# Kernel tuning notes

Hardware: AMD Instinct MI355X
Metric: run time of the kernel (lower is better)

The kernel has to match this reference:

```python
import jax, jax.numpy as jnp
import numpy as np

B, N, C, G, K = 4, 6000, 91, 32, 100
IMG = 800.0
SCORE_TH = 0.05
NMS_TH = 0.5
MATCH_TH = 0.5
MIN_SIZE = 0.01
BBOX_CLIP = float(np.log(1000.0 / 16.0))
WX, WY, WW, WH = 10.0, 10.0, 5.0, 5.0


def _make_boxes(key, shape_prefix):
    k1, k2 = jax.random.split(key)
    xy = jax.random.uniform(k1, shape_prefix + (2,), minval=0.0, maxval=IMG - 130.0)
    wh = jax.random.uniform(k2, shape_prefix + (2,), minval=8.0, maxval=128.0)
    return jnp.concatenate([xy, xy + wh], axis=-1)


def setup_inputs() -> dict:
    key = jax.random.key(0)
    k1, k2, k3, k4, k5 = jax.random.split(key, 5)
    return {
        "class_logits": 2.0 * jax.random.normal(k1, (B * N, C), dtype=jnp.float32),
        "box_regression": jax.random.normal(k2, (B * N, C * 4), dtype=jnp.float32),
        "proposals": _make_boxes(k3, (B, N)),
        "gt_boxes": _make_boxes(k4, (B, G)),
        "gt_labels": jax.random.randint(k5, (B, G), 1, C),
    }


def _box_iou(a, b):
    # a [G,4], b [N,4] -> [G,N]
    area_a = (a[:, 2] - a[:, 0]) * (a[:, 3] - a[:, 1])
    area_b = (b[:, 2] - b[:, 0]) * (b[:, 3] - b[:, 1])
    lt = jnp.maximum(a[:, None, :2], b[None, :, :2])
    rb = jnp.minimum(a[:, None, 2:], b[None, :, 2:])
    wh = jnp.clip(rb - lt, 0.0)
    inter = wh[..., 0] * wh[..., 1]
    return inter / (area_a[:, None] + area_b[None, :] - inter)


def _decode(rel, props):
    # torchvision BoxCoder.decode; rel [N,C,4], props [N,4]
    w = props[:, 2] - props[:, 0]
    h = props[:, 3] - props[:, 1]
    cx = props[:, 0] + 0.5 * w
    cy = props[:, 1] + 0.5 * h
    dx = rel[..., 0] / WX
    dy = rel[..., 1] / WY
    dw = jnp.minimum(rel[..., 2] / WW, BBOX_CLIP)
    dh = jnp.minimum(rel[..., 3] / WH, BBOX_CLIP)
    pcx = dx * w[:, None] + cx[:, None]
    pcy = dy * h[:, None] + cy[:, None]
    pw = jnp.exp(dw) * w[:, None]
    ph = jnp.exp(dh) * h[:, None]
    return jnp.stack([pcx - 0.5 * pw, pcy - 0.5 * ph, pcx + 0.5 * pw, pcy + 0.5 * ph], axis=-1)


def _image(logits, reg, props, gtb, gtl):
    # --- assign_targets_to_proposals (Matcher, low=high=0.5, no low-quality matches) ---
    iou = _box_iou(gtb, props)                      # [G, N]
    best = iou.max(axis=0)
    mi = jnp.argmax(iou, axis=0)
    matched = jnp.where(best >= MATCH_TH, mi, -1)   # -1 == BELOW_LOW_THRESHOLD
    assigned = jnp.where(matched >= 0, gtl[jnp.clip(matched, 0)], 0)

    # --- postprocess_detections ---
    scores = jax.nn.softmax(logits, axis=-1)[:, 1:].reshape(-1)                       # [N*(C-1)]
    boxes = jnp.clip(_decode(reg.reshape(N, C, 4), props)[:, 1:], 0.0, IMG)
    boxes = boxes.reshape(-1, 4)                                                      # [N*(C-1),4]
    labels = jnp.tile(jnp.arange(1, C), N)                                            # [N*(C-1)]
    ws = boxes[:, 2] - boxes[:, 0]
    hs = boxes[:, 3] - boxes[:, 1]
    valid = (scores > SCORE_TH) & (ws >= MIN_SIZE) & (hs >= MIN_SIZE)
    s0 = jnp.where(valid, scores, -jnp.inf)
    # batched_nms trick: offset boxes by label so cross-class IoU is 0
    off = boxes + (labels.astype(boxes.dtype) * (IMG + 1.0))[:, None]
    off_area = (off[:, 2] - off[:, 0]) * (off[:, 3] - off[:, 1])

    def step(s, _):
        i = jnp.argmax(s)
        sc = s[i]
        b = off[i]
        lt = jnp.maximum(off[:, :2], b[:2])
        rb = jnp.minimum(off[:, 2:], b[2:])
        wh = jnp.clip(rb - lt, 0.0)
        inter = wh[:, 0] * wh[:, 1]
        iou_all = inter / (off_area + (b[2] - b[0]) * (b[3] - b[1]) - inter)
        s = jnp.where(iou_all > NMS_TH, -jnp.inf, s)  # suppress (includes self)
        ok = jnp.isfinite(sc)
        ob = jnp.where(ok, boxes[i], 0.0)
        osc = jnp.where(ok, sc, 0.0)
        ol = jnp.where(ok, labels[i], -1)
        return s, (ob, osc, ol)

    _, (kb, ksc, kl) = jax.lax.scan(step, s0, None, length=K)
    return kb, ksc, kl, assigned, matched


def reference(class_logits, box_regression, proposals, gt_boxes, gt_labels):
    logits = class_logits.reshape(B, N, C)
    reg = box_regression.reshape(B, N, C * 4)
    kb, ksc, kl, assigned, matched = jax.vmap(_image)(logits, reg, proposals, gt_boxes, gt_labels)
    dets = jnp.concatenate([kb, ksc[..., None]], axis=-1)  # [B, K, 5]
    return dets, kl, assigned, matched
```

## Files before the change

kernel.cpp:

```cpp
#include <hip/hip_runtime.h>
#include <math.h>

#define NB 4
#define NN 6000
#define NC 91
#define NG 32
#define NK 100
#define NCLS (NC - 1)
#define NBUC (NB * NCLS)
#define SLOTS_MAX 2048
#define CUR_STRIDE 32
#define PMAX 512
#define MPB 4096
#define RS_BLOCKS 6000

#define SCORE_TH 0.05f
#define NMS_TH 0.5f
#define MATCH_TH 0.5f
#define MIN_SIZE 0.01f
#define BBOX_CLIP 4.135166556742356f
#define C_SUP 0.5000000298023223876953125

__device__ __forceinline__ bool decode_one(
    const float* __restrict__ reg, const float* __restrict__ props,
    float l, float m, float s0, int row, int c, float out[5])
{
    float score = __fdiv_rn(expf(__fsub_rn(l, m)), s0);

    const float4 p = *reinterpret_cast<const float4*>(props + (size_t)row * 4);
    float w  = __fsub_rn(p.z, p.x);
    float h  = __fsub_rn(p.w, p.y);
    float cx = __fadd_rn(p.x, __fmul_rn(0.5f, w));
    float cy = __fadd_rn(p.y, __fmul_rn(0.5f, h));

    const float4 r4 = *reinterpret_cast<const float4*>(
        reg + (size_t)row * (NC * 4) + (size_t)c * 4);
    float dx = __fdiv_rn(r4.x, 10.0f);
    float dy = __fdiv_rn(r4.y, 10.0f);
    float dw = fminf(__fdiv_rn(r4.z, 5.0f), BBOX_CLIP);
    float dh = fminf(__fdiv_rn(r4.w, 5.0f), BBOX_CLIP);

    float pcx = __fadd_rn(__fmul_rn(dx, w), cx);
    float pcy = __fadd_rn(__fmul_rn(dy, h), cy);
    float pw  = __fmul_rn(expf(dw), w);
    float ph  = __fmul_rn(expf(dh), h);

    float x1 = __fsub_rn(pcx, __fmul_rn(0.5f, pw));
    float y1 = __fsub_rn(pcy, __fmul_rn(0.5f, ph));
    float x2 = __fadd_rn(pcx, __fmul_rn(0.5f, pw));
    float y2 = __fadd_rn(pcy, __fmul_rn(0.5f, ph));
    x1 = fminf(fmaxf(x1, 0.0f), 800.0f);
    y1 = fminf(fmaxf(y1, 0.0f), 800.0f);
    x2 = fminf(fmaxf(x2, 0.0f), 800.0f);
    y2 = fminf(fmaxf(y2, 0.0f), 800.0f);

    out[0] = score; out[1] = x1; out[2] = y1; out[3] = x2; out[4] = y2;
    float ws_ = __fsub_rn(x2, x1);
    float hs_ = __fsub_rn(y2, y1);
    return (score > SCORE_TH) && (ws_ >= MIN_SIZE) && (hs_ >= MIN_SIZE);
}

__global__ __launch_bounds__(256) void fused_kernel(
    const float* __restrict__ logits, const float* __restrict__ reg,
    const float* __restrict__ props, const float* __restrict__ gtb,
    const int* __restrict__ gtl,
    float* __restrict__ out_assigned, float* __restrict__ out_matched,
    int* __restrict__ cursors,
    float* __restrict__ e_sc, float* __restrict__ e_x1,
    float* __restrict__ e_y1, float* __restrict__ e_x2,
    float* __restrict__ e_y2, float* __restrict__ e_id, int slots)
{
    int bid = blockIdx.x;
    if (bid < RS_BLOCKS) {
        int wid = threadIdx.x >> 6, lane = threadIdx.x & 63;
        int row = bid * 4 + wid;
        const float* rp = logits + (size_t)row * NC;
        float l0 = rp[lane];
        float l1 = (lane < NC - 64) ? rp[64 + lane] : -INFINITY;
        float m = fmaxf(fmaxf(-INFINITY, l0), l1);
        for (int o = 32; o; o >>= 1) m = fmaxf(m, __shfl_down(m, o));
        m = __shfl(m, 0);
        float s = __fadd_rn(__fadd_rn(0.0f, expf(__fsub_rn(l0, m))),
                            expf(__fsub_rn(l1, m)));
        for (int o = 32; o; o >>= 1) s = __fadd_rn(s, __shfl_down(s, o));
        float s0 = __shfl(s, 0);
        float thr = __fadd_rn(m, logf(__fmul_rn(0.04f, s0)));

        int b = row / NN;
        int nprop = row - b * NN;

        if (lane >= 1 && l0 > thr) {
            float o[5];
            if (decode_one(reg, props, l0, m, s0, row, lane, o)) {
                int c = lane;
                int g = b * NCLS + (c - 1);
                int pos = atomicAdd(&cursors[g * CUR_STRIDE], 1);
                if (pos < slots) {
                    size_t idx = (size_t)g * slots + pos;
                    e_sc[idx] = o[0]; e_x1[idx] = o[1]; e_y1[idx] = o[2];
                    e_x2[idx] = o[3]; e_y2[idx] = o[4];
                    e_id[idx] = (float)(nprop * NCLS + (c - 1));
                }
            }
        }
        if (lane < NC - 64 && l1 > thr) {
            float o[5];
            int c = lane + 64;
            if (decode_one(reg, props, l1, m, s0, row, c, o)) {
                int g = b * NCLS + (c - 1);
                int pos = atomicAdd(&cursors[g * CUR_STRIDE], 1);
                if (pos < slots) {
                    size_t idx = (size_t)g * slots + pos;
                    e_sc[idx] = o[0]; e_x1[idx] = o[1]; e_y1[idx] = o[2];
                    e_x2[idx] = o[3]; e_y2[idx] = o[4];
                    e_id[idx] = (float)(nprop * NCLS + (c - 1));
                }
            }
        }
    } else {
        int t = (bid - RS_BLOCKS) * 256 + threadIdx.x;
        if (t >= NB * NN) return;
        int b = t / NN;
        const float4 p = *reinterpret_cast<const float4*>(props + (size_t)t * 4);
        float parea = __fmul_rn(__fsub_rn(p.z, p.x), __fsub_rn(p.w, p.y));
        float best = -1.0f; int bi = -1;
        for (int g = 0; g < NG; ++g) {
            const float4 q = *reinterpret_cast<const float4*>(gtb + ((size_t)b * NG + g) * 4);
            float garea = __fmul_rn(__fsub_rn(q.z, q.x), __fsub_rn(q.w, q.y));
            float ltx = fmaxf(q.x, p.x), lty = fmaxf(q.y, p.y);
            float rbx = fminf(q.z, p.z), rby = fminf(q.w, p.w);
            float wx = fmaxf(__fsub_rn(rbx, ltx), 0.0f);
            float wy = fmaxf(__fsub_rn(rby, lty), 0.0f);
            float inter = __fmul_rn(wx, wy);
            float iou = __fdiv_rn(inter, __fsub_rn(__fadd_rn(garea, parea), inter));
            if (iou > best) { best = iou; bi = g; }
        }
        int matched = (best >= MATCH_TH) ? bi : -1;
        int assigned = (matched >= 0) ? gtl[b * NG + matched] : 0;
        out_matched[t]  = (float)matched;
        out_assigned[t] = (float)assigned;
    }
}

__device__ void nms_glb(int g, int n, float* __restrict__ SC,
                        const float* __restrict__ X1, const float* __restrict__ Y1,
                        const float* __restrict__ X2, const float* __restrict__ Y2,
                        const float* __restrict__ ID, float tb, float cls,
                        float* __restrict__ selbuf, int* __restrict__ selcnt)
{
    int lane = threadIdx.x;
    int kout = 0;
    for (int k = 0; k < NK; ++k) {
        float bv = -INFINITY, boi = INFINITY; int bi = -1;
        for (int i = lane; i < n; i += 64) {
            float v = SC[i], oi = ID[i];
            if (v > bv || (v == bv && oi < boi)) { bv = v; boi = oi; bi = i; }
        }
        int wl = lane;
        for (int o = 1; o < 64; o <<= 1) {
            float v2 = __shfl_xor(bv, o); float o2 = __shfl_xor(boi, o);
            int l2 = __shfl_xor(wl, o);
            bool bt = (v2 > bv) || (v2 == bv && o2 < boi);
            bv = bt ? v2 : bv; boi = bt ? o2 : boi; wl = bt ? l2 : wl;
        }
        if (bv == -INFINITY) break;
        int wi = __shfl(bi, wl);
        float sx1 = X1[wi], sy1 = Y1[wi], sx2 = X2[wi], sy2 = Y2[wi];
        if (lane == wl) {
            float* so = selbuf + ((size_t)g * NK + k) * 8;
            so[0] = bv; so[1] = sx1; so[2] = sy1; so[3] = sx2; so[4] = sy2;
            so[5] = cls; so[6] = boi; so[7] = 0.0f;
        }
        float bx1 = __fadd_rn(sx1, tb), by1 = __fadd_rn(sy1, tb);
        float bx2 = __fadd_rn(sx2, tb), by2 = __fadd_rn(sy2, tb);
        float sar = __fmul_rn(__fsub_rn(bx2, bx1), __fsub_rn(by2, by1));
        for (int i = lane; i < n; i += 64) {
            float v = SC[i];
            if (v == -INFINITY) continue;
            float ox1 = __fadd_rn(X1[i], tb), oy1 = __fadd_rn(Y1[i], tb);
            float ox2 = __fadd_rn(X2[i], tb), oy2 = __fadd_rn(Y2[i], tb);
            float oar = __fmul_rn(__fsub_rn(ox2, ox1), __fsub_rn(oy2, oy1));
            float ltx = fmaxf(ox1, bx1), lty = fmaxf(oy1, by1);
            float rbx = fminf(ox2, bx2), rby = fminf(oy2, by2);
            float wx = fmaxf(__fsub_rn(rbx, ltx), 0.0f);
            float wy = fmaxf(__fsub_rn(rby, lty), 0.0f);
            float inter = __fmul_rn(wx, wy);
            float den = __fsub_rn(__fadd_rn(oar, sar), inter);
            if ((double)inter > C_SUP * (double)den) SC[i] = -INFINITY;
        }
        kout = k + 1;
    }
    if (lane == 0) selcnt[g] = kout;
}

template <int CAP>
__device__ __forceinline__ float selN(const float a[CAP], int j) {
    float r = a[0];
#pragma unroll
    for (int i = 1; i < CAP; ++i) r = (j == i) ? a[i] : r;
    return r;
}
__device__ __forceinline__ float rdlane(float v, int l) {
    return __uint_as_float(
        (unsigned)__builtin_amdgcn_readlane((int)__float_as_uint(v), l));
}

template <int CAP>
__device__ __forceinline__ void sweep_reg(
    int lane, int n, float tb,
    const float* sx1, const float* sy1, const float* sx2, const float* sy2,
    int* acc, int* s_kout, int* selcnt, int g)
{
    float ox1[CAP], oy1[CAP], ox2[CAP], oy2[CAP], oar[CAP];
    unsigned alive = 0;
#pragma unroll
    for (int j = 0; j < CAP; ++j) {
        int sidx = lane * CAP + j;
        if (sidx < n) {
            float a  = __fadd_rn(sx1[sidx], tb);
            float b_ = __fadd_rn(sy1[sidx], tb);
            float c_ = __fadd_rn(sx2[sidx], tb);
            float d_ = __fadd_rn(sy2[sidx], tb);
            ox1[j] = a; oy1[j] = b_; ox2[j] = c_; oy2[j] = d_;
            oar[j] = __fmul_rn(__fsub_rn(c_, a), __fsub_rn(d_, b_));
            alive |= 1u << j;
        } else {
            ox1[j] = 0.f; oy1[j] = 0.f; ox2[j] = 0.f; oy2[j] = 0.f; oar[j] = 0.f;
        }
    }
    int kout = 0;
    while (kout < NK) {
        unsigned long long bal = __ballot(alive != 0u);
        if (!bal) break;
        int fl = (int)__ffsll(bal) - 1;
        unsigned am = (unsigned)__builtin_amdgcn_readlane((int)alive, fl);
        int js = __ffs(am) - 1;
        float bx1 = rdlane(selN<CAP>(ox1, js), fl);
        float by1 = rdlane(selN<CAP>(oy1, js), fl);
        float bx2 = rdlane(selN<CAP>(ox2, js), fl);
        float by2 = rdlane(selN<CAP>(oy2, js), fl);
        float bar = rdlane(selN<CAP>(oar, js), fl);
        if (lane == 0) acc[kout] = fl * CAP + js;
        kout++;
        unsigned kill = 0;
#pragma unroll
        for (int j = 0; j < CAP; ++j) {
            float ltx = fmaxf(ox1[j], bx1), lty = fmaxf(oy1[j], by1);
            float rbx = fminf(ox2[j], bx2), rby = fminf(oy2[j], by2);
            float wx = fmaxf(__fsub_rn(rbx, ltx), 0.0f);
            float wy = fmaxf(__fsub_rn(rby, lty), 0.0f);
            float inter = __fmul_rn(wx, wy);
            float den = __fsub_rn(__fadd_rn(oar[j], bar), inter);
            if ((double)inter > C_SUP * (double)den) kill |= 1u << j;
        }
        alive &= ~kill;
    }
    if (lane == 0) { selcnt[g] = kout; *s_kout = kout; }
}

__global__ __launch_bounds__(256) void bucket_nms_kernel(
    const int* __restrict__ cursors, int slots,
    float* __restrict__ e_sc, const float* __restrict__ e_x1,
    const float* __restrict__ e_y1, const float* __restrict__ e_x2,
    const float* __restrict__ e_y2, const float* __restrict__ e_id,
    float* __restrict__ selbuf, int* __restrict__ selcnt)
{
    int g = blockIdx.x;
    int n = cursors[g * CUR_STRIDE]; if (n > slots) n = slots;
    int tid = threadIdx.x;
    if (n == 0) { if (tid == 0) selcnt[g] = 0; return; }
    size_t base = (size_t)g * slots;
    float cls = (float)(g % NCLS + 1);
    float tb = __fmul_rn(cls, 801.0f);

    if (n > PMAX) {
        if (tid < 64)
            nms_glb(g, n, e_sc + base, e_x1 + base, e_y1 + base,
                    e_x2 + base, e_y2 + base, e_id + base, tb, cls,
                    selbuf, selcnt);
        return;
    }

    __shared__ unsigned skhi[PMAX], sklo[PMAX];
    __shared__ int sperm[PMAX];
    __shared__ float sx1[PMAX], sy1[PMAX], sx2[PMAX], sy2[PMAX];
    __shared__ int acc[NK];
    __shared__ int s_kout;

    int P = 64; while (P < n) P <<= 1;

    for (int i = tid; i < P; i += 256) {
        if (i < n) {
            skhi[i] = __float_as_uint(e_sc[base + i]);
            sklo[i] = ~((unsigned)e_id[base + i]);
        } else { skhi[i] = 0u; sklo[i] = 0u; }
        sperm[i] = i;
    }
    __syncthreads();
    for (int k = 2; k <= P; k <<= 1) {
        for (int j = k >> 1; j > 0; j >>= 1) {
            for (int t = tid; t < (P >> 1); t += 256) {
                int i = ((t & ~(j - 1)) << 1) | (t & (j - 1));
                int l = i | j;
                unsigned ah = skhi[i], al = sklo[i], ch = skhi[l], cl_ = sklo[l];
                bool alt = (ah < ch) || (ah == ch && al < cl_);
                bool agt = (ah > ch) || (ah == ch && al > cl_);
                bool sw = ((i & k) == 0) ? alt : agt;
                if (sw) {
                    skhi[i] = ch; sklo[i] = cl_; skhi[l] = ah; sklo[l] = al;
                    int tp = sperm[i]; sperm[i] = sperm[l]; sperm[l] = tp;
                }
            }
            __syncthreads();
        }
    }
    for (int i = tid; i < n; i += 256) {
        int sl = sperm[i];
        sx1[i] = e_x1[base + sl]; sy1[i] = e_y1[base + sl];
        sx2[i] = e_x2[base + sl]; sy2[i] = e_y2[base + sl];
    }
    __syncthreads();

    if (tid < 64) {
        if (n <= 256)
            sweep_reg<4>(tid, n, tb, sx1, sy1, sx2, sy2, acc, &s_kout, selcnt, g);
        else
            sweep_reg<8>(tid, n, tb, sx1, sy1, sx2, sy2, acc, &s_kout, selcnt, g);
    }
    __syncthreads();

    int kc = s_kout;
    for (int k = tid; k < kc; k += 256) {
        int cand = acc[k];
        float* so = selbuf + ((size_t)g * NK + k) * 8;
        so[0] = __uint_as_float(skhi[cand]);
        so[1] = sx1[cand]; so[2] = sy1[cand];
        so[3] = sx2[cand]; so[4] = sy2[cand];
        so[5] = cls; so[6] = (float)(~sklo[cand]); so[7] = 0.0f;
    }
}

__global__ __launch_bounds__(512) void merge_kernel(
    const float* __restrict__ selbuf, const int* __restrict__ selcnt,
    float* __restrict__ out_dets, float* __restrict__ out_kl)
{
    int b = blockIdx.x, tid = threadIdx.x;
    __shared__ int scnt[NCLS], soff[NCLS + 1];
    __shared__ unsigned akhi[512], aklo[512];
    __shared__ unsigned bkhi[MPB], bklo[MPB], bpay[MPB];
    __shared__ int s_T, s_cntA;
    __shared__ unsigned s_LBhi, s_LBlo;

    if (tid < NCLS) scnt[tid] = selcnt[b * NCLS + tid];
    if (tid == 0) s_T = 0;
    __syncthreads();
    if (tid == 0) {
        int a = 0, ca = 0;
        for (int c = 0; c < NCLS; ++c) {
            soff[c] = a; a += scnt[c];
            ca += (scnt[c] < 4 ? scnt[c] : 4);
        }
        soff[NCLS] = a; s_cntA = ca;
    }
    __syncthreads();
    int tot = soff[NCLS];

    if (tot == 0) {
        for (int z = tid; z < NK * 5; z += 512) out_dets[(size_t)b * NK * 5 + z] = 0.0f;
        for (int z = tid; z < NK; z += 512)     out_kl[(size_t)b * NK + z] = -1.0f;
        return;
    }

    {
        unsigned kh = 0u, kl = 0u;
        if (tid < NCLS * 4) {
            int c = tid >> 2, i = tid & 3;
            if (i < scnt[c]) {
                const float* e = selbuf + ((size_t)(b * NCLS + c) * NK + i) * 8;
                kh = __float_as_uint(e[0]); kl = ~((unsigned)e[6]);
            }
        }
        akhi[tid] = kh; aklo[tid] = kl;
    }
    __syncthreads();
    for (int k = 2; k <= 512; k <<= 1) {
        for (int j = k >> 1; j > 0; j >>= 1) {
            if (tid < 256) {
                int t = tid;
                int i = ((t & ~(j - 1)) << 1) | (t & (j - 1));
                int l = i | j;
                unsigned ah = akhi[i], al = aklo[i], ch = akhi[l], cl_ = aklo[l];
                bool alt = (ah < ch) || (ah == ch && al < cl_);
                bool agt = (ah > ch) || (ah == ch && al > cl_);
                bool sw = ((i & k) == 0) ? alt : agt;
                if (sw) {
                    akhi[i] = ch; aklo[i] = cl_; akhi[l] = ah; aklo[l] = al;
                }
            }
            __syncthreads();
        }
    }
    if (tid == 0) {
        if (s_cntA >= NK) { s_LBhi = akhi[NK - 1]; s_LBlo = aklo[NK - 1]; }
        else              { s_LBhi = 0u;           s_LBlo = 0u; }
    }
    __syncthreads();
    unsigned LBhi = s_LBhi, LBlo = s_LBlo;

    for (int flat = tid; flat < tot; flat += 512) {
        int lo = 0, hi = NCLS - 1;
        while (lo < hi) { int mid = (lo + hi + 1) >> 1;
                          if (soff[mid] <= flat) lo = mid; else hi = mid - 1; }
        int c = lo, i = flat - soff[c];
        const float* e = selbuf + ((size_t)(b * NCLS + c) * NK + i) * 8;
        unsigned kh = __float_as_uint(e[0]), kl = ~((unsigned)e[6]);
        bool ge = (kh > LBhi) || (kh == LBhi && kl >= LBlo);
        if (ge) {
            int pos = atomicAdd(&s_T, 1);
            if (pos < MPB) { bkhi[pos] = kh; bklo[pos] = kl;
                             bpay[pos] = (unsigned)((c << 7) | i); }
        }
    }
    __syncthreads();
    int T = s_T;

    if (T > MPB) {
        if (tid >= 64) return;
        int lane = tid;
        int g0 = b * NCLS + lane;
        int g1 = (lane < NCLS - 64) ? g0 + 64 : -1;
        int c0 = scnt[lane];
        int c1 = (g1 >= 0) ? scnt[lane + 64] : 0;
        int p0 = 0, p1 = 0;
        unsigned long long k0c = 0, k1c = 0;
        if (p0 < c0) { const float* h = selbuf + ((size_t)g0 * NK) * 8;
            k0c = ((unsigned long long)__float_as_uint(h[0]) << 32) | (unsigned long long)(~(unsigned)h[6]); }
        if (g1 >= 0 && p1 < c1) { const float* h = selbuf + ((size_t)g1 * NK) * 8;
            k1c = ((unsigned long long)__float_as_uint(h[0]) << 32) | (unsigned long long)(~(unsigned)h[6]); }
        for (int k = 0; k < NK; ++k) {
            bool t1 = (k1c > k0c);
            unsigned long long bk = t1 ? k1c : k0c;
            int bslot = t1 ? (lane + 64) : lane;
            for (int o = 1; o < 64; o <<= 1) {
                unsigned long long k2 = __shfl_xor(bk, o);
                int b2 = __shfl_xor(bslot, o);
                if (k2 > bk) { bk = k2; bslot = b2; }
            }
            if (bk == 0ull) {
                for (int z = k * 5 + lane; z < NK * 5; z += 64)
                    out_dets[(size_t)b * NK * 5 + z] = 0.0f;
                for (int z = k + lane; z < NK; z += 64)
                    out_kl[(size_t)b * NK + z] = -1.0f;
                return;
            }
            int owner = bslot & 63;
            if (lane == owner) {
                bool isA = (bslot < 64);
                int gg = isA ? g0 : g1;
                int pp = isA ? p0 : p1;
                const float* e = selbuf + ((size_t)gg * NK + pp) * 8;
                size_t o = ((size_t)b * NK + k) * 5;
                out_dets[o + 0] = e[1]; out_dets[o + 1] = e[2];
                out_dets[o + 2] = e[3]; out_dets[o + 3] = e[4];
                out_dets[o + 4] = e[0];
                out_kl[(size_t)b * NK + k] = e[5];
                if (isA) {
                    p0++; k0c = 0;
                    if (p0 < c0) { const float* h = selbuf + ((size_t)g0 * NK + p0) * 8;
                        k0c = ((unsigned long long)__float_as_uint(h[0]) << 32) | (unsigned long long)(~(unsigned)h[6]); }
                } else {
                    p1++; k1c = 0;
                    if (p1 < c1) { const float* h = selbuf + ((size_t)g1 * NK + p1) * 8;
                        k1c = ((unsigned long long)__float_as_uint(h[0]) << 32) | (unsigned long long)(~(unsigned)h[6]); }
                }
            }
        }
        return;
    }

    int P = 128; while (P < T) P <<= 1;
    for (int i = T + tid; i < P; i += 512) { bkhi[i] = 0u; bklo[i] = 0u; bpay[i] = 0u; }
    __syncthreads();
    for (int k = 2; k <= P; k <<= 1) {
        for (int j = k >> 1; j > 0; j >>= 1) {
            for (int t = tid; t < (P >> 1); t += 512) {
                int i = ((t & ~(j - 1)) << 1) | (t & (j - 1));
                int l = i | j;
                unsigned ah = bkhi[i], al = bklo[i], ch = bkhi[l], cl_ = bklo[l];
                bool alt = (ah < ch) || (ah == ch && al < cl_);
                bool agt = (ah > ch) || (ah == ch && al > cl_);
                bool sw = ((i & k) == 0) ? alt : agt;
                if (sw) {
                    bkhi[i] = ch; bklo[i] = cl_; bkhi[l] = ah; bklo[l] = al;
                    unsigned tp = bpay[i]; bpay[i] = bpay[l]; bpay[l] = tp;
                }
            }
            __syncthreads();
        }
    }
    int kc = (T < NK) ? T : NK;
    for (int k = tid; k < NK; k += 512) {
        size_t o = ((size_t)b * NK + k) * 5;
        if (k < kc) {
            unsigned pay = bpay[k];
            int c = (int)(pay >> 7), p = (int)(pay & 127);
            const float* e = selbuf + ((size_t)(b * NCLS + c) * NK + p) * 8;
            out_dets[o + 0] = e[1]; out_dets[o + 1] = e[2];
            out_dets[o + 2] = e[3]; out_dets[o + 3] = e[4];
            out_dets[o + 4] = e[0];
            out_kl[(size_t)b * NK + k] = e[5];
        } else {
            out_dets[o + 0] = 0.0f; out_dets[o + 1] = 0.0f;
            out_dets[o + 2] = 0.0f; out_dets[o + 3] = 0.0f;
            out_dets[o + 4] = 0.0f;
            out_kl[(size_t)b * NK + k] = -1.0f;
        }
    }
}

extern "C" void kernel_launch(void* const* d_in, const int* in_sizes, int n_in,
                              void* d_out, int out_size, void* d_ws, size_t ws_size,
                              hipStream_t stream) {
    const float* logits = (const float*)d_in[0];
    const float* reg    = (const float*)d_in[1];
    const float* props  = (const float*)d_in[2];
    const float* gtb    = (const float*)d_in[3];
    const int*   gtl    = (const int*)d_in[4];

    float* out          = (float*)d_out;
    float* out_dets     = out;
    float* out_kl       = out + NB * NK * 5;
    float* out_assigned = out_kl + NB * NK;
    float* out_matched  = out_assigned + NB * NN;

    char* ws = (char*)d_ws;
    int*   cursors = (int*)(ws + 0);
    int*   selcnt  = (int*)(ws + 49152);
    float* selbuf  = (float*)(ws + 53248);
    size_t off_ent = 1205248;

    long avail = (long)ws_size - (long)off_ent;
    long per_slot = 6L * 4L * NBUC;
    long slotsl = (avail > 0) ? avail / per_slot : 0;
    int slots = (int)((slotsl > SLOTS_MAX) ? SLOTS_MAX : (slotsl < 0 ? 0 : slotsl));

    size_t fsz = (size_t)NBUC * slots;
    float* e_sc = (float*)(ws + off_ent);
    float* e_x1 = e_sc + fsz;
    float* e_y1 = e_x1 + fsz;
    float* e_x2 = e_y1 + fsz;
    float* e_y2 = e_x2 + fsz;
    float* e_id = e_y2 + fsz;

    hipMemsetAsync(cursors, 0, NBUC * CUR_STRIDE * sizeof(int), stream);
    const int MATCH_BLOCKS = (NB * NN + 255) / 256;
    fused_kernel<<<RS_BLOCKS + MATCH_BLOCKS, 256, 0, stream>>>(
        logits, reg, props, gtb, gtl, out_assigned, out_matched,
        cursors, e_sc, e_x1, e_y1, e_x2, e_y2, e_id, slots);
    bucket_nms_kernel<<<NBUC, 256, 0, stream>>>(
        cursors, slots, e_sc, e_x1, e_y1, e_x2, e_y2, e_id, selbuf, selcnt);
    merge_kernel<<<NB, 512, 0, stream>>>(selbuf, selcnt, out_dets, out_kl);
}
```

Measured before the change: 127.9 us.

## Run per-bucket NMS kernel as a single wavefront without block barriers

Shrinks the bucket NMS kernel from 256 threads to one 64-lane wavefront. Block-wide __syncthreads between bitonic sort stages, the gather and the sweep are replaced with compiler scheduling barriers, relying on one wave's lockstep execution to order LDS accesses. The sweep now returns its keep count directly, so the shared s_kout variable goes away. The aim is to remove barrier and idle-wave overhead, especially since the sweep already ran on one wave, at the cost of each lane doing four times more sort and gather iterations.

```diff
diff --git a/kernel.cpp b/kernel.cpp
--- a/kernel.cpp
+++ b/kernel.cpp
@@ -148,7 +148,7 @@
                         const float* __restrict__ ID, float tb, float cls,
                         float* __restrict__ selbuf, int* __restrict__ selcnt)
 {
-    int lane = threadIdx.x;
+    int lane = threadIdx.x & 63;
     int kout = 0;
     for (int k = 0; k < NK; ++k) {
         float bv = -INFINITY, boi = INFINITY; int bi = -1;
@@ -206,10 +206,10 @@
 }
 
 template <int CAP>
-__device__ __forceinline__ void sweep_reg(
+__device__ __forceinline__ int sweep_reg(
     int lane, int n, float tb,
     const float* sx1, const float* sy1, const float* sx2, const float* sy2,
-    int* acc, int* s_kout, int* selcnt, int g)
+    int* acc)
 {
     float ox1[CAP], oy1[CAP], ox2[CAP], oy2[CAP], oar[CAP];
     unsigned alive = 0;
@@ -255,10 +255,10 @@
         }
         alive &= ~kill;
     }
-    if (lane == 0) { selcnt[g] = kout; *s_kout = kout; }
-}
-
-__global__ __launch_bounds__(256) void bucket_nms_kernel(
+    return kout;
+}
+
+__global__ __launch_bounds__(64) void bucket_nms_kernel(
     const int* __restrict__ cursors, int slots,
     float* __restrict__ e_sc, const float* __restrict__ e_x1,
     const float* __restrict__ e_y1, const float* __restrict__ e_x2,
@@ -267,17 +267,16 @@
 {
     int g = blockIdx.x;
     int n = cursors[g * CUR_STRIDE]; if (n > slots) n = slots;
-    int tid = threadIdx.x;
-    if (n == 0) { if (tid == 0) selcnt[g] = 0; return; }
+    int lane = threadIdx.x;
+    if (n == 0) { if (lane == 0) selcnt[g] = 0; return; }
     size_t base = (size_t)g * slots;
     float cls = (float)(g % NCLS + 1);
     float tb = __fmul_rn(cls, 801.0f);
 
     if (n > PMAX) {
-        if (tid < 64)
-            nms_glb(g, n, e_sc + base, e_x1 + base, e_y1 + base,
-                    e_x2 + base, e_y2 + base, e_id + base, tb, cls,
-                    selbuf, selcnt);
+        nms_glb(g, n, e_sc + base, e_x1 + base, e_y1 + base,
+                e_x2 + base, e_y2 + base, e_id + base, tb, cls,
+                selbuf, selcnt);
         return;
     }
 
@@ -285,21 +284,20 @@
     __shared__ int sperm[PMAX];
     __shared__ float sx1[PMAX], sy1[PMAX], sx2[PMAX], sy2[PMAX];
     __shared__ int acc[NK];
-    __shared__ int s_kout;
 
     int P = 64; while (P < n) P <<= 1;
 
-    for (int i = tid; i < P; i += 256) {
+    for (int i = lane; i < P; i += 64) {
         if (i < n) {
             skhi[i] = __float_as_uint(e_sc[base + i]);
             sklo[i] = ~((unsigned)e_id[base + i]);
         } else { skhi[i] = 0u; sklo[i] = 0u; }
         sperm[i] = i;
     }
-    __syncthreads();
+    __builtin_amdgcn_sched_barrier(0);
     for (int k = 2; k <= P; k <<= 1) {
         for (int j = k >> 1; j > 0; j >>= 1) {
-            for (int t = tid; t < (P >> 1); t += 256) {
+            for (int t = lane; t < (P >> 1); t += 64) {
                 int i = ((t & ~(j - 1)) << 1) | (t & (j - 1));
                 int l = i | j;
                 unsigned ah = skhi[i], al = sklo[i], ch = skhi[l], cl_ = sklo[l];
@@ -311,26 +309,25 @@
                     int tp = sperm[i]; sperm[i] = sperm[l]; sperm[l] = tp;
                 }
             }
-            __syncthreads();
-        }
-    }
-    for (int i = tid; i < n; i += 256) {
+            __builtin_amdgcn_sched_barrier(0);
+        }
+    }
+    for (int i = lane; i < n; i += 64) {
         int sl = sperm[i];
         sx1[i] = e_x1[base + sl]; sy1[i] = e_y1[base + sl];
         sx2[i] = e_x2[base + sl]; sy2[i] = e_y2[base + sl];
     }
-    __syncthreads();
-
-    if (tid < 64) {
-        if (n <= 256)
-            sweep_reg<4>(tid, n, tb, sx1, sy1, sx2, sy2, acc, &s_kout, selcnt, g);
-        else
-            sweep_reg<8>(tid, n, tb, sx1, sy1, sx2, sy2, acc, &s_kout, selcnt, g);
-    }
-    __syncthreads();
-
-    int kc = s_kout;
-    for (int k = tid; k < kc; k += 256) {
+    __builtin_amdgcn_sched_barrier(0);
+
+    int kout;
+    if (n <= 256)
+        kout = sweep_reg<4>(lane, n, tb, sx1, sy1, sx2, sy2, acc);
+    else
+        kout = sweep_reg<8>(lane, n, tb, sx1, sy1, sx2, sy2, acc);
+    if (lane == 0) selcnt[g] = kout;
+    __builtin_amdgcn_sched_barrier(0);
+
+    for (int k = lane; k < kout; k += 64) {
         int cand = acc[k];
         float* so = selbuf + ((size_t)g * NK + k) * 8;
         so[0] = __uint_as_float(skhi[cand]);
@@ -557,7 +554,7 @@
     fused_kernel<<<RS_BLOCKS + MATCH_BLOCKS, 256, 0, stream>>>(
         logits, reg, props, gtb, gtl, out_assigned, out_matched,
         cursors, e_sc, e_x1, e_y1, e_x2, e_y2, e_id, slots);
-    bucket_nms_kernel<<<NBUC, 256, 0, stream>>>(
+    bucket_nms_kernel<<<NBUC, 64, 0, stream>>>(
         cursors, slots, e_sc, e_x1, e_y1, e_x2, e_y2, e_id, selbuf, selcnt);
     merge_kernel<<<NB, 512, 0, stream>>>(selbuf, selcnt, out_dets, out_kl);
 }
```

Measured after the change: 148.3 us. +15.9%, slower.

## Pack bucket entries as AoS and use precomputed IoU bitmask NMS

Applied to the files above, without the earlier changes.

Candidate entries are now stored as 8-float records (box, score, id), written with vector stores instead of six scattered scalar arrays, and read back with float4 loads. The per-bucket NMS for small buckets now precomputes a pairwise suppression bitmask over the first 256 sorted candidates using all four waves, then does a cheap serial greedy sweep over the mask. The sequential register sweep remains only as a fallback when fewer than K boxes are kept and the bucket is larger than the mask width. Each entry now takes 32 bytes instead of 24, so fewer slots fit in the workspace, and the code adds shared memory for the mask.

```diff
diff --git a/kernel.cpp b/kernel.cpp
--- a/kernel.cpp
+++ b/kernel.cpp
@@ -11,6 +11,7 @@
 #define SLOTS_MAX 2048
 #define CUR_STRIDE 32
 #define PMAX 512
+#define MATW 256
 #define MPB 4096
 #define RS_BLOCKS 6000
 
@@ -65,10 +66,7 @@
     const float* __restrict__ props, const float* __restrict__ gtb,
     const int* __restrict__ gtl,
     float* __restrict__ out_assigned, float* __restrict__ out_matched,
-    int* __restrict__ cursors,
-    float* __restrict__ e_sc, float* __restrict__ e_x1,
-    float* __restrict__ e_y1, float* __restrict__ e_x2,
-    float* __restrict__ e_y2, float* __restrict__ e_id, int slots)
+    int* __restrict__ cursors, float* __restrict__ ent, int slots)
 {
     int bid = blockIdx.x;
     if (bid < RS_BLOCKS) {
@@ -96,10 +94,11 @@
                 int g = b * NCLS + (c - 1);
                 int pos = atomicAdd(&cursors[g * CUR_STRIDE], 1);
                 if (pos < slots) {
-                    size_t idx = (size_t)g * slots + pos;
-                    e_sc[idx] = o[0]; e_x1[idx] = o[1]; e_y1[idx] = o[2];
-                    e_x2[idx] = o[3]; e_y2[idx] = o[4];
-                    e_id[idx] = (float)(nprop * NCLS + (c - 1));
+                    float* e = ent + ((size_t)g * slots + pos) * 8;
+                    *reinterpret_cast<float4*>(e) =
+                        make_float4(o[1], o[2], o[3], o[4]);
+                    *reinterpret_cast<float2*>(e + 4) =
+                        make_float2(o[0], (float)(nprop * NCLS + (c - 1)));
                 }
             }
         }
@@ -110,10 +109,11 @@
                 int g = b * NCLS + (c - 1);
                 int pos = atomicAdd(&cursors[g * CUR_STRIDE], 1);
                 if (pos < slots) {
-                    size_t idx = (size_t)g * slots + pos;
-                    e_sc[idx] = o[0]; e_x1[idx] = o[1]; e_y1[idx] = o[2];
-                    e_x2[idx] = o[3]; e_y2[idx] = o[4];
-                    e_id[idx] = (float)(nprop * NCLS + (c - 1));
+                    float* e = ent + ((size_t)g * slots + pos) * 8;
+                    *reinterpret_cast<float4*>(e) =
+                        make_float4(o[1], o[2], o[3], o[4]);
+                    *reinterpret_cast<float2*>(e + 4) =
+                        make_float2(o[0], (float)(nprop * NCLS + (c - 1)));
                 }
             }
         }
@@ -142,18 +142,15 @@
     }
 }
 
-__device__ void nms_glb(int g, int n, float* __restrict__ SC,
-                        const float* __restrict__ X1, const float* __restrict__ Y1,
-                        const float* __restrict__ X2, const float* __restrict__ Y2,
-                        const float* __restrict__ ID, float tb, float cls,
+__device__ void nms_glb(int g, int n, float* __restrict__ E, float tb, float cls,
                         float* __restrict__ selbuf, int* __restrict__ selcnt)
 {
-    int lane = threadIdx.x;
+    int lane = threadIdx.x & 63;
     int kout = 0;
     for (int k = 0; k < NK; ++k) {
         float bv = -INFINITY, boi = INFINITY; int bi = -1;
         for (int i = lane; i < n; i += 64) {
-            float v = SC[i], oi = ID[i];
+            float v = E[(size_t)i * 8 + 4], oi = E[(size_t)i * 8 + 5];
             if (v > bv || (v == bv && oi < boi)) { bv = v; boi = oi; bi = i; }
         }
         int wl = lane;
@@ -165,7 +162,8 @@
         }
         if (bv == -INFINITY) break;
         int wi = __shfl(bi, wl);
-        float sx1 = X1[wi], sy1 = Y1[wi], sx2 = X2[wi], sy2 = Y2[wi];
+        float sx1 = E[(size_t)wi * 8 + 0], sy1 = E[(size_t)wi * 8 + 1];
+        float sx2 = E[(size_t)wi * 8 + 2], sy2 = E[(size_t)wi * 8 + 3];
         if (lane == wl) {
             float* so = selbuf + ((size_t)g * NK + k) * 8;
             so[0] = bv; so[1] = sx1; so[2] = sy1; so[3] = sx2; so[4] = sy2;
@@ -175,10 +173,12 @@
         float bx2 = __fadd_rn(sx2, tb), by2 = __fadd_rn(sy2, tb);
         float sar = __fmul_rn(__fsub_rn(bx2, bx1), __fsub_rn(by2, by1));
         for (int i = lane; i < n; i += 64) {
-            float v = SC[i];
+            float v = E[(size_t)i * 8 + 4];
             if (v == -INFINITY) continue;
-            float ox1 = __fadd_rn(X1[i], tb), oy1 = __fadd_rn(Y1[i], tb);
-            float ox2 = __fadd_rn(X2[i], tb), oy2 = __fadd_rn(Y2[i], tb);
+            float ox1 = __fadd_rn(E[(size_t)i * 8 + 0], tb);
+            float oy1 = __fadd_rn(E[(size_t)i * 8 + 1], tb);
+            float ox2 = __fadd_rn(E[(size_t)i * 8 + 2], tb);
+            float oy2 = __fadd_rn(E[(size_t)i * 8 + 3], tb);
             float oar = __fmul_rn(__fsub_rn(ox2, ox1), __fsub_rn(oy2, oy1));
             float ltx = fmaxf(ox1, bx1), lty = fmaxf(oy1, by1);
             float rbx = fminf(ox2, bx2), rby = fminf(oy2, by2);
@@ -186,7 +186,7 @@
             float wy = fmaxf(__fsub_rn(rby, lty), 0.0f);
             float inter = __fmul_rn(wx, wy);
             float den = __fsub_rn(__fadd_rn(oar, sar), inter);
-            if ((double)inter > C_SUP * (double)den) SC[i] = -INFINITY;
+            if ((double)inter > C_SUP * (double)den) E[(size_t)i * 8 + 4] = -INFINITY;
         }
         kout = k + 1;
     }
@@ -206,10 +206,10 @@
 }
 
 template <int CAP>
-__device__ __forceinline__ void sweep_reg(
+__device__ __forceinline__ int sweep_reg(
     int lane, int n, float tb,
     const float* sx1, const float* sy1, const float* sx2, const float* sy2,
-    int* acc, int* s_kout, int* selcnt, int g)
+    int* acc)
 {
     float ox1[CAP], oy1[CAP], ox2[CAP], oy2[CAP], oar[CAP];
     unsigned alive = 0;
@@ -255,44 +255,41 @@
         }
         alive &= ~kill;
     }
-    if (lane == 0) { selcnt[g] = kout; *s_kout = kout; }
+    return kout;
 }
 
 __global__ __launch_bounds__(256) void bucket_nms_kernel(
     const int* __restrict__ cursors, int slots,
-    float* __restrict__ e_sc, const float* __restrict__ e_x1,
-    const float* __restrict__ e_y1, const float* __restrict__ e_x2,
-    const float* __restrict__ e_y2, const float* __restrict__ e_id,
+    float* __restrict__ entries,
     float* __restrict__ selbuf, int* __restrict__ selcnt)
 {
     int g = blockIdx.x;
     int n = cursors[g * CUR_STRIDE]; if (n > slots) n = slots;
     int tid = threadIdx.x;
     if (n == 0) { if (tid == 0) selcnt[g] = 0; return; }
-    size_t base = (size_t)g * slots;
+    float* E = entries + (size_t)g * slots * 8;
     float cls = (float)(g % NCLS + 1);
     float tb = __fmul_rn(cls, 801.0f);
 
     if (n > PMAX) {
-        if (tid < 64)
-            nms_glb(g, n, e_sc + base, e_x1 + base, e_y1 + base,
-                    e_x2 + base, e_y2 + base, e_id + base, tb, cls,
-                    selbuf, selcnt);
+        if (tid < 64) nms_glb(g, n, E, tb, cls, selbuf, selcnt);
         return;
     }
 
     __shared__ unsigned skhi[PMAX], sklo[PMAX];
     __shared__ int sperm[PMAX];
     __shared__ float sx1[PMAX], sy1[PMAX], sx2[PMAX], sy2[PMAX];
+    __shared__ unsigned long long dmask[MATW * 4];
     __shared__ int acc[NK];
-    __shared__ int s_kout;
+    __shared__ int s_kout, s_fb;
 
     int P = 64; while (P < n) P <<= 1;
 
     for (int i = tid; i < P; i += 256) {
         if (i < n) {
-            skhi[i] = __float_as_uint(e_sc[base + i]);
-            sklo[i] = ~((unsigned)e_id[base + i]);
+            const float* e = E + (size_t)i * 8;
+            skhi[i] = __float_as_uint(e[4]);
+            sklo[i] = ~((unsigned)e[5]);
         } else { skhi[i] = 0u; sklo[i] = 0u; }
         sperm[i] = i;
     }
@@ -315,21 +312,96 @@
         }
     }
     for (int i = tid; i < n; i += 256) {
-        int sl = sperm[i];
-        sx1[i] = e_x1[base + sl]; sy1[i] = e_y1[base + sl];
-        sx2[i] = e_x2[base + sl]; sy2[i] = e_y2[base + sl];
+        const float4 v = *reinterpret_cast<const float4*>(E + (size_t)sperm[i] * 8);
+        sx1[i] = v.x; sy1[i] = v.y; sx2[i] = v.z; sy2[i] = v.w;
+    }
+    __syncthreads();
+
+    int W = (n < MATW) ? n : MATW;
+    int nchunk = (W + 63) >> 6;
+    int wv = tid >> 6, lane = tid & 63;
+
+    float jx1[4], jy1[4], jx2[4], jy2[4], jar[4];
+#pragma unroll
+    for (int c = 0; c < 4; ++c) {
+        int j = c * 64 + lane;
+        if (j < W) {
+            float a  = __fadd_rn(sx1[j], tb);
+            float b_ = __fadd_rn(sy1[j], tb);
+            float c_ = __fadd_rn(sx2[j], tb);
+            float d_ = __fadd_rn(sy2[j], tb);
+            jx1[c] = a; jy1[c] = b_; jx2[c] = c_; jy2[c] = d_;
+            jar[c] = __fmul_rn(__fsub_rn(c_, a), __fsub_rn(d_, b_));
+        } else {
+            jx1[c] = 0.f; jy1[c] = 0.f; jx2[c] = 0.f; jy2[c] = 0.f; jar[c] = 0.f;
+        }
+    }
+    {
+        int i0 = wv;
+        float nx1 = 0.f, ny1 = 0.f, nx2 = 0.f, ny2 = 0.f;
+        if (i0 < W) { nx1 = sx1[i0]; ny1 = sy1[i0]; nx2 = sx2[i0]; ny2 = sy2[i0]; }
+        for (int i = i0; i < W; i += 4) {
+            float rx1 = nx1, ry1 = ny1, rx2 = nx2, ry2 = ny2;
+            int ni = i + 4;
+            if (ni < W) { nx1 = sx1[ni]; ny1 = sy1[ni]; nx2 = sx2[ni]; ny2 = sy2[ni]; }
+            float bx1 = __fadd_rn(rx1, tb), by1 = __fadd_rn(ry1, tb);
+            float bx2 = __fadd_rn(rx2, tb), by2 = __fadd_rn(ry2, tb);
+            float bar = __fmul_rn(__fsub_rn(bx2, bx1), __fsub_rn(by2, by1));
+            int ic = i >> 6;
+#pragma unroll
+            for (int c = 0; c < 4; ++c) {
+                if (c >= ic && c < nchunk) {
+                    bool jv = (c * 64 + lane) < W;
+                    float ltx = fmaxf(jx1[c], bx1), lty = fmaxf(jy1[c], by1);
+                    float rbx = fminf(jx2[c], bx2), rby = fminf(jy2[c], by2);
+                    float wx = fmaxf(__fsub_rn(rbx, ltx), 0.0f);
+                    float wy = fmaxf(__fsub_rn(rby, lty), 0.0f);
+                    float inter = __fmul_rn(wx, wy);
+                    float den = __fsub_rn(__fadd_rn(jar[c], bar), inter);
+                    bool sup = jv && ((double)inter > C_SUP * (double)den);
+                    unsigned long long w64 = __ballot(sup);
+                    if (lane == 0) dmask[i * 4 + c] = w64;
+                }
+            }
+        }
     }
     __syncthreads();
 
     if (tid < 64) {
-        if (n <= 256)
-            sweep_reg<4>(tid, n, tb, sx1, sy1, sx2, sy2, acc, &s_kout, selcnt, g);
-        else
-            sweep_reg<8>(tid, n, tb, sx1, sy1, sx2, sy2, acc, &s_kout, selcnt, g);
-    }
-    __syncthreads();
+        unsigned long long alive = 0ull;
+        if (lane < nchunk) {
+            int rem = W - (lane << 6);
+            alive = (rem >= 64) ? ~0ull : ((1ull << rem) - 1ull);
+        }
+        int kout = 0;
+        while (kout < NK) {
+            unsigned long long bal = __ballot(alive != 0ull);
+            if (!bal) break;
+            int fl = (int)__ffsll(bal) - 1;
+            unsigned long long am = __shfl(alive, fl);
+            int js = (int)__ffsll(am) - 1;
+            int cand = (fl << 6) + js;
+            if (lane == 0) acc[kout] = cand;
+            kout++;
+            if (lane < nchunk) alive &= ~dmask[cand * 4 + lane];
+        }
+        if (lane == 0) {
+            s_kout = kout;
+            s_fb = (kout < NK && n > W) ? 1 : 0;
+        }
+    }
+    __syncthreads();
+
+    if (s_fb) {
+        if (tid < 64) {
+            int kout = sweep_reg<8>(lane, n, tb, sx1, sy1, sx2, sy2, acc);
+            if (lane == 0) s_kout = kout;
+        }
+        __syncthreads();
+    }
 
     int kc = s_kout;
+    if (tid == 0) selcnt[g] = kc;
     for (int k = tid; k < kc; k += 256) {
         int cand = acc[k];
         float* so = selbuf + ((size_t)g * NK + k) * 8;
@@ -540,24 +612,18 @@
     size_t off_ent = 1205248;
 
     long avail = (long)ws_size - (long)off_ent;
-    long per_slot = 6L * 4L * NBUC;
+    long per_slot = 32L * NBUC;
     long slotsl = (avail > 0) ? avail / per_slot : 0;
     int slots = (int)((slotsl > SLOTS_MAX) ? SLOTS_MAX : (slotsl < 0 ? 0 : slotsl));
 
-    size_t fsz = (size_t)NBUC * slots;
-    float* e_sc = (float*)(ws + off_ent);
-    float* e_x1 = e_sc + fsz;
-    float* e_y1 = e_x1 + fsz;
-    float* e_x2 = e_y1 + fsz;
-    float* e_y2 = e_x2 + fsz;
-    float* e_id = e_y2 + fsz;
+    float* entries = (float*)(ws + off_ent);
 
     hipMemsetAsync(cursors, 0, NBUC * CUR_STRIDE * sizeof(int), stream);
     const int MATCH_BLOCKS = (NB * NN + 255) / 256;
     fused_kernel<<<RS_BLOCKS + MATCH_BLOCKS, 256, 0, stream>>>(
         logits, reg, props, gtb, gtl, out_assigned, out_matched,
-        cursors, e_sc, e_x1, e_y1, e_x2, e_y2, e_id, slots);
+        cursors, entries, slots);
     bucket_nms_kernel<<<NBUC, 256, 0, stream>>>(
-        cursors, slots, e_sc, e_x1, e_y1, e_x2, e_y2, e_id, selbuf, selcnt);
+        cursors, slots, entries, selbuf, selcnt);
     merge_kernel<<<NB, 512, 0, stream>>>(selbuf, selcnt, out_dets, out_kl);
 }
```

After: 121.5 us. -5.0%, faster.
